# Kernel optimization log

Measured on AMD Instinct MI355X. Metric: run time of the kernel, lower is better.

The kernel has to match this reference:

```python
import jax, jax.numpy as jnp
import numpy as np

B, S, SE, D, H, FF, E, K = 2, 2048, 2048, 1024, 16, 4096, 8, 2
HD = D // H


def setup_inputs() -> dict:
    key = jax.random.key(0)
    ks = jax.random.split(key, 32)
    w = lambda k, shape: jax.random.normal(k, shape, jnp.float32) * 0.02
    inp = {
        'x': jax.random.normal(ks[0], (B, S, D), jnp.float32),
        'encoder_output': jax.random.normal(ks[1], (B, SE, D), jnp.float32),
        # causal self-attention projections
        'sa_wq': w(ks[2], (D, D)), 'sa_bq': jnp.zeros((D,), jnp.float32),
        'sa_wk': w(ks[3], (D, D)), 'sa_bk': jnp.zeros((D,), jnp.float32),
        'sa_wv': w(ks[4], (D, D)), 'sa_bv': jnp.zeros((D,), jnp.float32),
        'sa_wo': w(ks[5], (D, D)), 'sa_bo': jnp.zeros((D,), jnp.float32),
        # cross-attention projections
        'ca_wq': w(ks[6], (D, D)), 'ca_bq': jnp.zeros((D,), jnp.float32),
        'ca_wk': w(ks[7], (D, D)), 'ca_bk': jnp.zeros((D,), jnp.float32),
        'ca_wv': w(ks[8], (D, D)), 'ca_bv': jnp.zeros((D,), jnp.float32),
        'ca_wo': w(ks[9], (D, D)), 'ca_bo': jnp.zeros((D,), jnp.float32),
        # layernorms
        'ln1_g': jnp.ones((D,), jnp.float32), 'ln1_b': jnp.zeros((D,), jnp.float32),
        'ln2_g': jnp.ones((D,), jnp.float32), 'ln2_b': jnp.zeros((D,), jnp.float32),
        'ln3_g': jnp.ones((D,), jnp.float32), 'ln3_b': jnp.zeros((D,), jnp.float32),
        # router + experts
        'router_w': w(ks[10], (D, E)), 'router_b': jnp.zeros((E,), jnp.float32),
        'e_w1': w(ks[11], (E, D, FF)), 'e_b1': jnp.zeros((E, FF), jnp.float32),
        'e_w2': w(ks[12], (E, FF, D)), 'e_b2': jnp.zeros((E, D), jnp.float32),
    }
    return inp


def _layernorm(x, g, b):
    m = x.mean(-1, keepdims=True)
    v = ((x - m) ** 2).mean(-1, keepdims=True)
    return (x - m) / jnp.sqrt(v + 1e-5) * g + b


def _attn(q_in, k_in, v_in, wq, bq, wk, bk, wv, bv, wo, bo, causal):
    Bq, Sq, Dm = q_in.shape
    Sk = k_in.shape[1]
    Q = (q_in @ wq + bq).reshape(Bq, Sq, H, HD)
    Kp = (k_in @ wk + bk).reshape(Bq, Sk, H, HD)
    V = (v_in @ wv + bv).reshape(Bq, Sk, H, HD)
    scores = jnp.einsum('bqhd,bkhd->bhqk', Q, Kp) / jnp.sqrt(jnp.float32(HD))
    if causal:
        mask = jnp.tril(jnp.ones((Sq, Sk), bool))
        scores = jnp.where(mask, scores, -jnp.inf)
    a = jax.nn.softmax(scores, axis=-1)
    o = jnp.einsum('bhqk,bkhd->bqhd', a, V).reshape(Bq, Sq, Dm)
    return o @ wo + bo


def _moe(x, rw, rb, w1, b1, w2, b2):
    T = x.shape[0] * x.shape[1]
    xf = x.reshape(T, D)
    router_weights = jax.nn.softmax(xf @ rw + rb, axis=-1)          # [T,E]
    topw, topi = jax.lax.top_k(router_weights, K)                   # [T,K]
    topw = jax.nn.softmax(topw, axis=-1)                            # renormalize top-k
    # combine[t,e] = sum_k topw[t,k] * (topi[t,k]==e)
    combine = jnp.zeros((T, E), xf.dtype).at[jnp.arange(T)[:, None], topi].add(topw)
    # dense compute over all experts (same math as masked dispatch)
    h = jax.nn.gelu(jnp.einsum('td,edf->etf', xf, w1) + b1[:, None, :], approximate=False)
    eo = jnp.einsum('etf,efd->etd', h, w2) + b2[:, None, :]          # [E,T,D]
    out = jnp.einsum('etd,te->td', eo, combine)
    return out.reshape(x.shape)


def reference(x, encoder_output,
              sa_wq, sa_bq, sa_wk, sa_bk, sa_wv, sa_bv, sa_wo, sa_bo,
              ca_wq, ca_bq, ca_wk, ca_bk, ca_wv, ca_bv, ca_wo, ca_bo,
              ln1_g, ln1_b, ln2_g, ln2_b, ln3_g, ln3_b,
              router_w, router_b, e_w1, e_b1, e_w2, e_b2):
    x = _layernorm(x + _attn(x, x, x, sa_wq, sa_bq, sa_wk, sa_bk, sa_wv, sa_bv, sa_wo, sa_bo, True), ln1_g, ln1_b)
    x = _layernorm(x + _attn(x, encoder_output, encoder_output, ca_wq, ca_bq, ca_wk, ca_bk, ca_wv, ca_bv, ca_wo, ca_bo, False), ln2_g, ln2_b)
    x = _layernorm(x + _moe(x, router_w, router_b, e_w1, e_b1, e_w2, e_b2), ln3_g, ln3_b)
    return x
```

## Files before the change

### kernel.cpp

```cpp
#include <hip/hip_runtime.h>

typedef unsigned short u16;
typedef unsigned int   u32;
typedef __bf16    bf16x8 __attribute__((ext_vector_type(8)));
typedef _Float16  f16x8  __attribute__((ext_vector_type(8)));
typedef __fp16    fp16x2 __attribute__((ext_vector_type(2)));
typedef float     f32x4  __attribute__((ext_vector_type(4)));
typedef u16       u16x4  __attribute__((ext_vector_type(4)));

#define DEV static __device__ __forceinline__

constexpr int DIMc  = 1024;
constexpr int NHEAD = 16;
constexpr int HDM   = 64;
constexpr int SLENc = 2048;
constexpr int NBAT  = 2;
constexpr int NTOK  = NBAT * SLENc;
constexpr int FFD   = 4096;
constexpr int NEXP  = 8;
constexpr int NSLOT = 2 * NTOK;
constexpr long TD   = (long)NTOK * DIMc;
constexpr float RSC = 2048.0f;
constexpr float RSCI = 1.0f / 2048.0f;

DEV u16 f2bf(float f) {
  u32 u = __float_as_uint(f);
  u += 0x7fffu + ((u >> 16) & 1u);
  return (u16)(u >> 16);
}
DEV float bf2f(u16 h) { return __uint_as_float(((u32)h) << 16); }
DEV float h2f(u16 u) { union { _Float16 h; u16 u_; } x; x.u_ = u; return (float)x.h; }

DEV void split2v(float v, u16& h, u16& r) {
  _Float16 hh = (_Float16)v;
  float rf = (v - (float)hh) * RSC;
  union { _Float16 h_; u16 u_; } a, b;
  a.h_ = hh; b.h_ = (_Float16)rf;
  h = a.u_; r = b.u_;
}

DEV u32 pkrtz(float a, float b) {
  union { fp16x2 v; u32 u; } x;
  x.v = __builtin_amdgcn_cvt_pkrtz(a, b);
  return x.u;
}

DEV void async16(const void* g, void* l) {
  __builtin_amdgcn_global_load_lds((const u32*)g, (u32*)l, 16, 0, 0);
}

DEV f32x4 mfma_bf(bf16x8 a, bf16x8 b, f32x4 c) {
  return __builtin_amdgcn_mfma_f32_16x16x32_bf16(a, b, c, 0, 0, 0);
}
DEV f32x4 mfma_h(f16x8 a, f16x8 b, f32x4 c) {
  return __builtin_amdgcn_mfma_f32_16x16x32_f16(a, b, c, 0, 0, 0);
}

DEV f16x8 ldfragh(const u16 (*T)[64], int row, int blk) {
  return *(const f16x8*)((const u16*)T + row * 64 + ((blk ^ (row & 7)) * 8));
}

__global__ __launch_bounds__(256) void split2_kernel(
    const float* __restrict__ x, u16* __restrict__ o0, u16* __restrict__ o1, long n) {
  long i = ((long)blockIdx.x * 256 + threadIdx.x) * 4;
  if (i >= n) return;
  f32x4 v = *(const f32x4*)(x + i);
  u16x4 h, r;
#pragma unroll
  for (int j = 0; j < 4; ++j) { u16 a, b; split2v(v[j], a, b); h[j] = a; r[j] = b; }
  *(u16x4*)(o0 + i) = h;
  *(u16x4*)(o1 + i) = r;
}

__global__ __launch_bounds__(256) void wsplit2_kernel(
    const float* __restrict__ W, u16* __restrict__ t0, u16* __restrict__ t1, int R, int C) {
  __shared__ alignas(16) float tile[32][33];
  const long base = (long)blockIdx.z * R * C;
  const int c0 = blockIdx.x * 32, r0 = blockIdx.y * 32;
  const int tx = threadIdx.x & 31, ty = threadIdx.x >> 5;
#pragma unroll
  for (int i = 0; i < 32; i += 8)
    tile[ty + i][tx] = W[base + (long)(r0 + ty + i) * C + (c0 + tx)];
  __syncthreads();
#pragma unroll
  for (int i = 0; i < 32; i += 8) {
    float v = tile[tx][ty + i];
    long oidx = base + (long)(c0 + ty + i) * R + (r0 + tx);
    u16 a, b; split2v(v, a, b);
    t0[oidx] = a; t1[oidx] = b;
  }
}

__global__ __launch_bounds__(256) void wsplit1_kernel(
    const float* __restrict__ W, u16* __restrict__ t0, int R, int C) {
  __shared__ alignas(16) float tile[32][33];
  const long base = (long)blockIdx.z * R * C;
  const int c0 = blockIdx.x * 32, r0 = blockIdx.y * 32;
  const int tx = threadIdx.x & 31, ty = threadIdx.x >> 5;
#pragma unroll
  for (int i = 0; i < 32; i += 8)
    tile[ty + i][tx] = W[base + (long)(r0 + ty + i) * C + (c0 + tx)];
  __syncthreads();
#pragma unroll
  for (int i = 0; i < 32; i += 8) {
    long oidx = base + (long)(c0 + ty + i) * R + (r0 + tx);
    t0[oidx] = f2bf(tile[tx][ty + i]);
  }
}

__global__ __launch_bounds__(256) void biascat_kernel(
    const float* __restrict__ q, const float* __restrict__ k, const float* __restrict__ v,
    const float* __restrict__ ck, const float* __restrict__ cv,
    float* __restrict__ qkvb, float* __restrict__ kvb) {
  int i = blockIdx.x * 256 + threadIdx.x;
  if (i < 1024) qkvb[i] = q[i];
  else if (i < 2048) qkvb[i] = k[i - 1024];
  else if (i < 3072) qkvb[i] = v[i - 2048];
  else if (i < 4096) kvb[i - 3072] = ck[i - 3072];
  else if (i < 5120) kvb[i - 3072] = cv[i - 4096];
}

__global__ __launch_bounds__(256) void vtrans2_kernel(
    const u16* __restrict__ vh, const u16* __restrict__ vr, int ld,
    u16* __restrict__ t0, u16* __restrict__ t1) {
  __shared__ alignas(16) float tile[32][33];
  const int bh = blockIdx.z, b = bh >> 4, h = bh & 15;
  const int s0 = blockIdx.x * 32, d0 = blockIdx.y * 32;
  const int tx = threadIdx.x & 31, ty = threadIdx.x >> 5;
#pragma unroll
  for (int i = 0; i < 32; i += 8) {
    long idx = (long)(b * SLENc + s0 + ty + i) * ld + h * HDM + d0 + tx;
    tile[ty + i][tx] = h2f(vh[idx]) + h2f(vr[idx]) * RSCI;
  }
  __syncthreads();
#pragma unroll
  for (int i = 0; i < 32; i += 8) {
    float v = tile[tx][ty + i];
    long o = ((long)bh * HDM + d0 + ty + i) * SLENc + s0 + tx;
    u16 a, b_; split2v(v, a, b_);
    t0[o] = a; t1[o] = b_;
  }
}

template<int BK, bool SPLIT, bool GATHER, int EPI>
__global__ __launch_bounds__(256) void gemm_kernel(
    const u16* __restrict__ A0, const u16* __restrict__ A1,
    const u16* __restrict__ B0, const u16* __restrict__ B1,
    const float* __restrict__ bias, void* __restrict__ Cout, u16* __restrict__ C1,
    int M, int N, int Kd,
    const int* __restrict__ tlist, const int* __restrict__ cnts, const int* __restrict__ offs) {
  constexpr int NP = SPLIT ? 2 : 1;
  constexpr int NCH = (BK == 32) ? 2 : 4;
  __shared__ alignas(16) u16 As[NP][128 * BK];
  __shared__ alignas(16) u16 Bs[NP][128 * BK];

  const int e   = blockIdx.z;
  const int cnt = cnts ? cnts[e] : M;
  const int off = offs ? offs[e] : 0;
  const int m0  = blockIdx.y * 128;
  if (m0 >= cnt) return;
  const int n0  = blockIdx.x * 128;

  const int tid = threadIdx.x;
  const int lane = tid & 63, wid = tid >> 6;
  const int fr = lane & 15, kc = lane >> 4;
  const int wr = wid >> 1, wc = wid & 1;

  const long boff = (long)e * N * Kd;

  long arow_off[NCH], brow_off[NCH];
#pragma unroll
  for (int c = 0; c < NCH; ++c) {
    int row, kseg8;
    if constexpr (BK == 32) {
      const int chunk = wid * 2 + c;
      row = chunk * 16 + (lane >> 2);
      kseg8 = lane & 3;
    } else {
      const int chunk = wid * 4 + c;
      const int srow8 = lane >> 3;
      row = chunk * 8 + srow8;
      kseg8 = (lane & 7) ^ (srow8 & 7);
    }
    long ar;
    if (GATHER) {
      int idx = m0 + row; if (idx >= cnt) idx = cnt - 1;
      ar = tlist[off + idx];
    } else {
      ar = (long)(off + m0 + row);
    }
    arow_off[c] = ar * Kd + kseg8 * 8;
    brow_off[c] = boff + (long)(n0 + row) * Kd + kseg8 * 8;
  }

  f32x4 acc[4][4], acc1[4][4];
#pragma unroll
  for (int m = 0; m < 4; ++m)
#pragma unroll
    for (int n = 0; n < 4; ++n) { acc[m][n] = f32x4{0.f,0.f,0.f,0.f}; acc1[m][n] = f32x4{0.f,0.f,0.f,0.f}; }

  const int NK = Kd / BK;
  for (int kt = 0; kt < NK; ++kt) {
    const int k0 = kt * BK;
    __syncthreads();
#pragma unroll
    for (int c = 0; c < NCH; ++c) {
      const int chunk = wid * NCH + c;
      async16(A0 + arow_off[c] + k0, &As[0][chunk * 512]);
      async16(B0 + brow_off[c] + k0, &Bs[0][chunk * 512]);
      if constexpr (SPLIT) {
        async16(A1 + arow_off[c] + k0, &As[1][chunk * 512]);
        async16(B1 + brow_off[c] + k0, &Bs[1][chunk * 512]);
      }
    }
    __syncthreads();

    if constexpr (BK == 32) {
      if constexpr (SPLIT) {
        f16x8 a0[4], a1[4];
#pragma unroll
        for (int m = 0; m < 4; ++m) {
          const int idx = (wr * 64 + m * 16 + fr) * 32 + kc * 8;
          a0[m] = *(const f16x8*)&As[0][idx];
          a1[m] = *(const f16x8*)&As[1][idx];
        }
#pragma unroll
        for (int n = 0; n < 4; ++n) {
          const int idx = (wc * 64 + n * 16 + fr) * 32 + kc * 8;
          f16x8 b0 = *(const f16x8*)&Bs[0][idx];
          f16x8 b1 = *(const f16x8*)&Bs[1][idx];
#pragma unroll
          for (int m = 0; m < 4; ++m) {
            acc[m][n]  = mfma_h(a0[m], b0, acc[m][n]);
            acc1[m][n] = mfma_h(a0[m], b1, acc1[m][n]);
            acc1[m][n] = mfma_h(a1[m], b0, acc1[m][n]);
          }
        }
      } else {
        bf16x8 a0[4];
#pragma unroll
        for (int m = 0; m < 4; ++m)
          a0[m] = *(const bf16x8*)&As[0][(wr * 64 + m * 16 + fr) * 32 + kc * 8];
#pragma unroll
        for (int n = 0; n < 4; ++n) {
          bf16x8 b0 = *(const bf16x8*)&Bs[0][(wc * 64 + n * 16 + fr) * 32 + kc * 8];
#pragma unroll
          for (int m = 0; m < 4; ++m)
            acc[m][n] = mfma_bf(a0[m], b0, acc[m][n]);
        }
      }
    } else {
#pragma unroll
      for (int ksub = 0; ksub < 2; ++ksub) {
        bf16x8 a0[4];
#pragma unroll
        for (int m = 0; m < 4; ++m) {
          const int row = wr * 64 + m * 16 + fr;
          a0[m] = *(const bf16x8*)&As[0][row * 64 + (((ksub << 2) | kc) ^ (fr & 7)) * 8];
        }
#pragma unroll
        for (int n = 0; n < 4; ++n) {
          const int row = wc * 64 + n * 16 + fr;
          bf16x8 b0 = *(const bf16x8*)&Bs[0][row * 64 + (((ksub << 2) | kc) ^ (fr & 7)) * 8];
#pragma unroll
          for (int m = 0; m < 4; ++m)
            acc[m][n] = mfma_bf(a0[m], b0, acc[m][n]);
        }
      }
    }
  }

  const float* bvec = bias + (long)e * N;
#pragma unroll
  for (int m = 0; m < 4; ++m) {
#pragma unroll
    for (int j = 0; j < 4; ++j) {
      const int r = m0 + wr * 64 + m * 16 + (lane >> 4) * 4 + j;
      if (r >= cnt) continue;
      const long orow = (long)(off + r) * N;
#pragma unroll
      for (int n = 0; n < 4; ++n) {
        const int col = n0 + wc * 64 + n * 16 + fr;
        float v = acc[m][n][j];
        if constexpr (SPLIT) v += acc1[m][n][j] * RSCI;
        v += bvec[col];
        if constexpr (EPI == 0) {
          ((float*)Cout)[orow + col] = v;
        } else if constexpr (EPI == 1) {
          float g = 0.5f * v * (1.0f + erff(v * 0.70710678118654752f));
          ((u16*)Cout)[orow + col] = f2bf(g);
        } else if constexpr (EPI == 2) {
          ((u16*)Cout)[orow + col] = f2bf(v);
        } else {
          u16 a_, b_; split2v(v, a_, b_);
          ((u16*)Cout)[orow + col] = a_;
          C1[orow + col] = b_;
        }
      }
    }
  }
}

DEV f16x8 gather_fragh(u32 a0, u32 a1, u32 b0, u32 b1, int lane) {
  const int kc = lane >> 4;
  const int base = (lane & 15) + ((kc & 1) << 5);
  union { u32 u[4]; f16x8 v; } r;
  u32 s00 = (u32)__shfl((int)a0, base, 64);
  u32 s01 = (u32)__shfl((int)a1, base, 64);
  u32 s10 = (u32)__shfl((int)b0, base, 64);
  u32 s11 = (u32)__shfl((int)b1, base, 64);
  u32 t00 = (u32)__shfl((int)a0, base + 16, 64);
  u32 t01 = (u32)__shfl((int)a1, base + 16, 64);
  u32 t10 = (u32)__shfl((int)b0, base + 16, 64);
  u32 t11 = (u32)__shfl((int)b1, base + 16, 64);
  const bool hi = (kc >> 1) != 0;
  r.u[0] = hi ? s10 : s00;
  r.u[1] = hi ? s11 : s01;
  r.u[2] = hi ? t10 : t00;
  r.u[3] = hi ? t11 : t01;
  return r.v;
}

template<bool CAUSAL>
__global__ __launch_bounds__(256, 3) void attn2_kernel(
    const u16* __restrict__ Qh, const u16* __restrict__ Qr, int qld,
    const u16* __restrict__ Kh, const u16* __restrict__ Kr, int kld,
    const u16* __restrict__ Vh, const u16* __restrict__ Vr,
    u16* __restrict__ OH, u16* __restrict__ OR) {
  __shared__ alignas(16) u16 KQs[2][64][64];
  __shared__ alignas(16) u16 Vts[2][64][64];

  const int qt = blockIdx.x, h = blockIdx.y, b = blockIdx.z;
  const int tid = threadIdx.x, lane = tid & 63, w = tid >> 6;
  const int fr = lane & 15, kc = lane >> 4;
  const int q0 = qt * 64;
  const long qbase = (long)(b * SLENc) * qld + h * HDM;
  const long kbase = (long)(b * SLENc) * kld + h * HDM;
  const long obase = (long)(b * SLENc) * DIMc + h * HDM;
  const long vtbase = (long)(b * NHEAD + h) * HDM * SLENc;
  const int r = lane >> 3, blk = (lane & 7) ^ r;

#pragma unroll
  for (int p = 0; p < 2; ++p) {
    const u16* gp = (p == 0 ? Qh : Qr);
#pragma unroll
    for (int cc = 0; cc < 2; ++cc) {
      int c = w + 4 * cc;
      async16(gp + qbase + (long)(q0 + 8 * c + r) * qld + blk * 8, &KQs[p][8 * c][0]);
    }
  }
  __syncthreads();
  f16x8 qf0[2], qf1[2];
#pragma unroll
  for (int s = 0; s < 2; ++s) {
    qf0[s] = ldfragh(KQs[0], w * 16 + fr, s * 4 + kc);
    qf1[s] = ldfragh(KQs[1], w * 16 + fr, s * 4 + kc);
  }
  __syncthreads();

  f32x4 accO0[4], accO1[4];
#pragma unroll
  for (int dn = 0; dn < 4; ++dn) { accO0[dn] = f32x4{0.f,0.f,0.f,0.f}; accO1[dn] = f32x4{0.f,0.f,0.f,0.f}; }
  float m_ = -3e38f, l_ = 0.f;

  const int nkt = CAUSAL ? (qt + 1) : (SLENc / 64);
  for (int kt = 0; kt < nkt; ++kt) {
    __syncthreads();
    {
#pragma unroll
      for (int p = 0; p < 2; ++p) {
        const u16* gp = (p == 0 ? Kh : Kr);
#pragma unroll
        for (int cc = 0; cc < 2; ++cc) {
          int c = w + 4 * cc;
          async16(gp + kbase + (long)(kt * 64 + 8 * c + r) * kld + blk * 8, &KQs[p][8 * c][0]);
        }
      }
      const long vrow = vtbase + kt * 64;
#pragma unroll
      for (int p = 0; p < 2; ++p) {
        const u16* gp = (p == 0 ? Vh : Vr);
#pragma unroll
        for (int cc = 0; cc < 2; ++cc) {
          int c = w + 4 * cc;
          async16(gp + vrow + (long)(8 * c + r) * SLENc + blk * 8, &Vts[p][8 * c][0]);
        }
      }
    }
    __syncthreads();

    f32x4 sc0[4], sc1[4];
#pragma unroll
    for (int kn = 0; kn < 4; ++kn) { sc0[kn] = f32x4{0.f,0.f,0.f,0.f}; sc1[kn] = f32x4{0.f,0.f,0.f,0.f}; }
#pragma unroll
    for (int kn = 0; kn < 4; ++kn)
#pragma unroll
      for (int s = 0; s < 2; ++s) {
        f16x8 ah = ldfragh(KQs[0], kn * 16 + fr, s * 4 + kc);
        f16x8 ar = ldfragh(KQs[1], kn * 16 + fr, s * 4 + kc);
        sc0[kn] = mfma_h(ah, qf0[s], sc0[kn]);
        sc1[kn] = mfma_h(ah, qf1[s], sc1[kn]);
        sc1[kn] = mfma_h(ar, qf0[s], sc1[kn]);
      }

    constexpr float SCL = 0.125f, SCL2 = 0.125f * RSCI;
    float p_[4][4];
    float mx = -3e38f;
#pragma unroll
    for (int kn = 0; kn < 4; ++kn)
#pragma unroll
      for (int j = 0; j < 4; ++j) {
        float sv = fmaf(sc0[kn][j], SCL, sc1[kn][j] * SCL2);
        if (CAUSAL && kt == qt) {
          if (kn * 16 + kc * 4 + j > w * 16 + fr) sv = -3e38f;
        }
        p_[kn][j] = sv;
        mx = fmaxf(mx, sv);
      }
    mx = fmaxf(mx, __shfl_xor(mx, 16, 64));
    mx = fmaxf(mx, __shfl_xor(mx, 32, 64));
    if (!__all(mx <= m_ + 8.f)) {
      const float mn = fmaxf(m_, mx);
      const float corr = __expf(m_ - mn);
      m_ = mn;
      l_ *= corr;
#pragma unroll
      for (int dn = 0; dn < 4; ++dn) { accO0[dn] *= corr; accO1[dn] *= corr; }
    }
    float rs = 0.f;
#pragma unroll
    for (int kn = 0; kn < 4; ++kn)
#pragma unroll
      for (int j = 0; j < 4; ++j) {
        float p = __expf(p_[kn][j] - m_);
        p_[kn][j] = p;
        rs += p;
      }
    rs += __shfl_xor(rs, 16, 64);
    rs += __shfl_xor(rs, 32, 64);
    l_ += rs;

    u32 hpk[4][2], rpk[4][2];
#pragma unroll
    for (int kn = 0; kn < 4; ++kn)
#pragma unroll
      for (int jp = 0; jp < 2; ++jp) {
        float p0 = p_[kn][2 * jp], p1 = p_[kn][2 * jp + 1];
        u32 hp = pkrtz(p0, p1);
        float h0 = h2f((u16)hp), h1 = h2f((u16)(hp >> 16));
        u32 rp = pkrtz((p0 - h0) * RSC, (p1 - h1) * RSC);
        hpk[kn][jp] = hp;
        rpk[kn][jp] = rp;
      }

#pragma unroll
    for (int s = 0; s < 2; ++s) {
      f16x8 ph = gather_fragh(hpk[2 * s][0], hpk[2 * s][1], hpk[2 * s + 1][0], hpk[2 * s + 1][1], lane);
      f16x8 pr = gather_fragh(rpk[2 * s][0], rpk[2 * s][1], rpk[2 * s + 1][0], rpk[2 * s + 1][1], lane);
#pragma unroll
      for (int dn = 0; dn < 4; ++dn) {
        f16x8 vh = ldfragh(Vts[0], dn * 16 + fr, s * 4 + kc);
        f16x8 vr = ldfragh(Vts[1], dn * 16 + fr, s * 4 + kc);
        accO0[dn] = mfma_h(vh, ph, accO0[dn]);
        accO1[dn] = mfma_h(vh, pr, accO1[dn]);
        accO1[dn] = mfma_h(vr, ph, accO1[dn]);
      }
    }
  }

  const float inv = 1.0f / l_;
#pragma unroll
  for (int dn = 0; dn < 4; ++dn) {
    u16x4 hv, rv;
#pragma unroll
    for (int j = 0; j < 4; ++j) {
      float o = (accO0[dn][j] + accO1[dn][j] * RSCI) * inv;
      u16 a_, b_; split2v(o, a_, b_);
      hv[j] = a_; rv[j] = b_;
    }
    const long oidx = obase + (long)(q0 + w * 16 + fr) * DIMc + dn * 16 + kc * 4;
    *(u16x4*)&OH[oidx] = hv;
    *(u16x4*)&OR[oidx] = rv;
  }
}

template<int NS>
__global__ __launch_bounds__(256) void resln_kernel(
    const float* __restrict__ resid, const float* __restrict__ proj,
    const float* __restrict__ gam, const float* __restrict__ bet,
    float* __restrict__ yout, u16* __restrict__ s0, u16* __restrict__ s1) {
  __shared__ float red[4];
  const int t = blockIdx.x, tid = threadIdx.x;
  const long base = (long)t * DIMc;
  float v[4];
#pragma unroll
  for (int i = 0; i < 4; ++i) {
    int d = tid + i * 256;
    v[i] = resid[base + d] + proj[base + d];
  }
  float s = v[0] + v[1] + v[2] + v[3];
#pragma unroll
  for (int o = 32; o; o >>= 1) s += __shfl_xor(s, o, 64);
  if ((tid & 63) == 0) red[tid >> 6] = s;
  __syncthreads();
  const float mean = (red[0] + red[1] + red[2] + red[3]) * (1.0f / DIMc);
  __syncthreads();
  float q = 0.f;
#pragma unroll
  for (int i = 0; i < 4; ++i) { float d_ = v[i] - mean; q += d_ * d_; }
#pragma unroll
  for (int o = 32; o; o >>= 1) q += __shfl_xor(q, o, 64);
  if ((tid & 63) == 0) red[tid >> 6] = q;
  __syncthreads();
  const float var = (red[0] + red[1] + red[2] + red[3]) * (1.0f / DIMc);
  const float inv = rsqrtf(var + 1e-5f);
#pragma unroll
  for (int i = 0; i < 4; ++i) {
    int d = tid + i * 256;
    float y = (v[i] - mean) * inv * gam[d] + bet[d];
    yout[base + d] = y;
    if constexpr (NS == 1) s0[base + d] = f2bf(y);
    if constexpr (NS == 2) {
      u16 a, b; split2v(y, a, b);
      s0[base + d] = a; s1[base + d] = b;
    }
  }
}

__global__ __launch_bounds__(256) void router_kernel(
    const float* __restrict__ x2, const float* __restrict__ rw, const float* __restrict__ rb,
    int* __restrict__ topi, float* __restrict__ topw, int* __restrict__ cnt) {
  const int t = blockIdx.x * 4 + (threadIdx.x >> 6);
  const int lane = threadIdx.x & 63;
  float a[8] = {};
  for (int it = 0; it < 16; ++it) {
    int d = it * 64 + lane;
    float xv = x2[(long)t * DIMc + d];
    const f32x4* wp = (const f32x4*)&rw[d * 8];
    f32x4 w0 = wp[0], w1 = wp[1];
    a[0] += xv * w0[0]; a[1] += xv * w0[1]; a[2] += xv * w0[2]; a[3] += xv * w0[3];
    a[4] += xv * w1[0]; a[5] += xv * w1[1]; a[6] += xv * w1[2]; a[7] += xv * w1[3];
  }
#pragma unroll
  for (int o = 32; o; o >>= 1)
#pragma unroll
    for (int e = 0; e < 8; ++e) a[e] += __shfl_xor(a[e], o, 64);
  if (lane == 0) {
    float lg[8];
#pragma unroll
    for (int e = 0; e < 8; ++e) lg[e] = a[e] + rb[e];
    int i1 = 0;
#pragma unroll
    for (int e = 1; e < 8; ++e) if (lg[e] > lg[i1]) i1 = e;
    int i2 = (i1 == 0) ? 1 : 0;
#pragma unroll
    for (int e = 0; e < 8; ++e) if (e != i1 && lg[e] > lg[i2]) i2 = e;
    float mx = lg[i1], ps = 0.f, p[8];
#pragma unroll
    for (int e = 0; e < 8; ++e) { p[e] = __expf(lg[e] - mx); ps += p[e]; }
    float p1 = p[i1] / ps, p2 = p[i2] / ps;
    float e2 = __expf(p2 - p1);
    float w1 = 1.0f / (1.0f + e2);
    topi[t * 2] = i1; topi[t * 2 + 1] = i2;
    topw[t * 2] = w1; topw[t * 2 + 1] = e2 * w1;
    atomicAdd(&cnt[i1], 1); atomicAdd(&cnt[i2], 1);
  }
}

__global__ void scan_kernel(const int* __restrict__ cnt, int* __restrict__ offs, int* __restrict__ pos) {
  if (threadIdx.x == 0) {
    int a = 0;
    for (int e = 0; e < NEXP; ++e) { offs[e] = a; a += cnt[e]; }
  }
  if (threadIdx.x < NEXP) pos[threadIdx.x] = 0;
}

__global__ __launch_bounds__(256) void fill_kernel(
    const int* __restrict__ topi, const int* __restrict__ offs, int* __restrict__ pos,
    int* __restrict__ tlist, int* __restrict__ slotof) {
  int t = blockIdx.x * 256 + threadIdx.x;
  if (t >= NTOK) return;
#pragma unroll
  for (int k = 0; k < 2; ++k) {
    int e = topi[t * 2 + k];
    int pp = atomicAdd(&pos[e], 1);
    int s = offs[e] + pp;
    tlist[s] = t;
    slotof[t * 2 + k] = s;
  }
}

__global__ __launch_bounds__(256) void final_kernel(
    const float* __restrict__ x2, const u16* __restrict__ eo,
    const int* __restrict__ slotof, const float* __restrict__ topw,
    const float* __restrict__ gam, const float* __restrict__ bet, float* __restrict__ out) {
  __shared__ float red[4];
  const int t = blockIdx.x, tid = threadIdx.x;
  const long base = (long)t * DIMc;
  const int s0 = slotof[t * 2], s1 = slotof[t * 2 + 1];
  const float w0 = topw[t * 2], w1 = topw[t * 2 + 1];
  float v[4];
#pragma unroll
  for (int i = 0; i < 4; ++i) {
    int d = tid + i * 256;
    float moe = w0 * bf2f(eo[(long)s0 * DIMc + d]) + w1 * bf2f(eo[(long)s1 * DIMc + d]);
    v[i] = x2[base + d] + moe;
  }
  float s = v[0] + v[1] + v[2] + v[3];
#pragma unroll
  for (int o = 32; o; o >>= 1) s += __shfl_xor(s, o, 64);
  if ((tid & 63) == 0) red[tid >> 6] = s;
  __syncthreads();
  const float mean = (red[0] + red[1] + red[2] + red[3]) * (1.0f / DIMc);
  __syncthreads();
  float q = 0.f;
#pragma unroll
  for (int i = 0; i < 4; ++i) { float d_ = v[i] - mean; q += d_ * d_; }
#pragma unroll
  for (int o = 32; o; o >>= 1) q += __shfl_xor(q, o, 64);
  if ((tid & 63) == 0) red[tid >> 6] = q;
  __syncthreads();
  const float var = (red[0] + red[1] + red[2] + red[3]) * (1.0f / DIMc);
  const float inv = rsqrtf(var + 1e-5f);
#pragma unroll
  for (int i = 0; i < 4; ++i) {
    int d = tid + i * 256;
    out[base + d] = (v[i] - mean) * inv * gam[d] + bet[d];
  }
}

extern "C" void kernel_launch(void* const* d_in, const int* in_sizes, int n_in,
                              void* d_out, int out_size, void* d_ws, size_t ws_size,
                              hipStream_t stream) {
  (void)in_sizes; (void)n_in; (void)out_size; (void)ws_size;
  const float* x     = (const float*)d_in[0];
  const float* enc   = (const float*)d_in[1];
  const float* aw[8] = {(const float*)d_in[2],  (const float*)d_in[4],  (const float*)d_in[6],  (const float*)d_in[8],
                        (const float*)d_in[10], (const float*)d_in[12], (const float*)d_in[14], (const float*)d_in[16]};
  const float* ab[8] = {(const float*)d_in[3],  (const float*)d_in[5],  (const float*)d_in[7],  (const float*)d_in[9],
                        (const float*)d_in[11], (const float*)d_in[13], (const float*)d_in[15], (const float*)d_in[17]};
  const float* ln1_g = (const float*)d_in[18]; const float* ln1_b = (const float*)d_in[19];
  const float* ln2_g = (const float*)d_in[20]; const float* ln2_b = (const float*)d_in[21];
  const float* ln3_g = (const float*)d_in[22]; const float* ln3_b = (const float*)d_in[23];
  const float* rw    = (const float*)d_in[24]; const float* rb    = (const float*)d_in[25];
  const float* e_w1  = (const float*)d_in[26]; const float* e_b1  = (const float*)d_in[27];
  const float* e_w2  = (const float*)d_in[28]; const float* e_b2  = (const float*)d_in[29];

  char* basep = (char*)d_ws;
  size_t offb = 0;
  auto alloc = [&](size_t nbytes) -> void* {
    void* r = basep + offb;
    offb += (nbytes + 255) & ~(size_t)255;
    return r;
  };

  const size_t PLANE_BF = (size_t)TD * 2;
  const size_t PLANE_F  = (size_t)TD * 4;
  const size_t WPLANE   = (size_t)DIMc * DIMc * 2;

  u16 *xs0 = (u16*)alloc(PLANE_BF), *xs1 = (u16*)alloc(PLANE_BF);
  u16 *es0 = (u16*)alloc(PLANE_BF), *es1 = (u16*)alloc(PLANE_BF);
  u16 *os0 = (u16*)alloc(PLANE_BF), *os1 = (u16*)alloc(PLANE_BF);
  u16 *wqkv0 = (u16*)alloc(3 * WPLANE), *wqkv1 = (u16*)alloc(3 * WPLANE);
  u16 *wkv0  = (u16*)alloc(2 * WPLANE), *wkv1  = (u16*)alloc(2 * WPLANE);
  u16 *wq0   = (u16*)alloc(WPLANE),     *wq1   = (u16*)alloc(WPLANE);
  u16 *wo10  = (u16*)alloc(WPLANE),     *wo11  = (u16*)alloc(WPLANE);
  u16 *wo20  = (u16*)alloc(WPLANE),     *wo21  = (u16*)alloc(WPLANE);
  u16* w1t = (u16*)alloc((size_t)NEXP * FFD * DIMc * 2);
  u16* w2t = (u16*)alloc((size_t)NEXP * DIMc * FFD * 2);
  u16 *QKVh = (u16*)alloc(3 * PLANE_BF), *QKVr = (u16*)alloc(3 * PLANE_BF);
  u16 *KVh  = (u16*)alloc(2 * PLANE_BF), *KVr  = (u16*)alloc(2 * PLANE_BF);
  u16 *Qch  = (u16*)alloc(PLANE_BF),     *Qcr  = (u16*)alloc(PLANE_BF);
  u16 *Vth  = (u16*)alloc(PLANE_BF),     *Vtr  = (u16*)alloc(PLANE_BF);
  float* qkvb = (float*)alloc(3072 * 4);
  float* kvb  = (float*)alloc(2048 * 4);
  float* aout = (float*)alloc(PLANE_F);
  float* x1   = (float*)alloc(PLANE_F);
  float* x2   = (float*)alloc(PLANE_F);
  u16*   x2h  = (u16*)alloc(PLANE_BF);
  u16*   hbuf = (u16*)alloc((size_t)(NSLOT + 128) * FFD * 2);
  u16*   eo   = (u16*)alloc((size_t)NSLOT * DIMc * 2);
  int*   topi   = (int*)alloc(NSLOT * 4);
  float* topwp  = (float*)alloc(NSLOT * 4);
  int*   tlist  = (int*)alloc(NSLOT * 4);
  int*   slotof = (int*)alloc(NSLOT * 4);
  int*   cnt    = (int*)alloc(NEXP * 4);
  int*   offs   = (int*)alloc(NEXP * 4);
  int*   pos    = (int*)alloc(NEXP * 4);

  (void)hipMemsetAsync(cnt, 0, NEXP * sizeof(int), stream);

  const int SB = (int)(TD / 4 / 256);
  split2_kernel<<<SB, 256, 0, stream>>>(x, xs0, xs1, TD);
  split2_kernel<<<SB, 256, 0, stream>>>(enc, es0, es1, TD);
  for (int s = 0; s < 3; ++s)
    wsplit2_kernel<<<dim3(32, 32, 1), 256, 0, stream>>>(aw[s], wqkv0 + (size_t)s * DIMc * DIMc, wqkv1 + (size_t)s * DIMc * DIMc, DIMc, DIMc);
  wsplit2_kernel<<<dim3(32, 32, 1), 256, 0, stream>>>(aw[5], wkv0, wkv1, DIMc, DIMc);
  wsplit2_kernel<<<dim3(32, 32, 1), 256, 0, stream>>>(aw[6], wkv0 + (size_t)DIMc * DIMc, wkv1 + (size_t)DIMc * DIMc, DIMc, DIMc);
  wsplit2_kernel<<<dim3(32, 32, 1), 256, 0, stream>>>(aw[4], wq0, wq1, DIMc, DIMc);
  wsplit2_kernel<<<dim3(32, 32, 1), 256, 0, stream>>>(aw[3], wo10, wo11, DIMc, DIMc);
  wsplit2_kernel<<<dim3(32, 32, 1), 256, 0, stream>>>(aw[7], wo20, wo21, DIMc, DIMc);
  wsplit1_kernel<<<dim3(FFD / 32, DIMc / 32, NEXP), 256, 0, stream>>>(e_w1, w1t, DIMc, FFD);
  wsplit1_kernel<<<dim3(DIMc / 32, FFD / 32, NEXP), 256, 0, stream>>>(e_w2, w2t, FFD, DIMc);
  biascat_kernel<<<20, 256, 0, stream>>>(ab[0], ab[1], ab[2], ab[5], ab[6], qkvb, kvb);

  const dim3 gproj(DIMc / 128, NTOK / 128, 1);
  const dim3 gqkv(3 * DIMc / 128, NTOK / 128, 1);
  const dim3 gkv(2 * DIMc / 128, NTOK / 128, 1);
  const dim3 gattn(SLENc / 64, NHEAD, NBAT);
  const dim3 gvt(SLENc / 32, HDM / 32, NBAT * NHEAD);

  gemm_kernel<32, true, false, 3><<<gqkv, 256, 0, stream>>>(xs0, xs1, wqkv0, wqkv1, qkvb, QKVh, QKVr, NTOK, 3 * DIMc, DIMc, nullptr, nullptr, nullptr);
  vtrans2_kernel<<<gvt, 256, 0, stream>>>(QKVh + 2048, QKVr + 2048, 3 * DIMc, Vth, Vtr);
  attn2_kernel<true><<<gattn, 256, 0, stream>>>(QKVh, QKVr, 3 * DIMc, QKVh + 1024, QKVr + 1024, 3 * DIMc, Vth, Vtr, os0, os1);
  gemm_kernel<32, true, false, 0><<<gproj, 256, 0, stream>>>(os0, os1, wo10, wo11, ab[3], aout, nullptr, NTOK, DIMc, DIMc, nullptr, nullptr, nullptr);
  resln_kernel<2><<<NTOK, 256, 0, stream>>>(x, aout, ln1_g, ln1_b, x1, xs0, xs1);
  gemm_kernel<32, true, false, 3><<<gproj, 256, 0, stream>>>(xs0, xs1, wq0, wq1, ab[4], Qch, Qcr, NTOK, DIMc, DIMc, nullptr, nullptr, nullptr);
  gemm_kernel<32, true, false, 3><<<gkv, 256, 0, stream>>>(es0, es1, wkv0, wkv1, kvb, KVh, KVr, NTOK, 2 * DIMc, DIMc, nullptr, nullptr, nullptr);
  vtrans2_kernel<<<gvt, 256, 0, stream>>>(KVh + 1024, KVr + 1024, 2 * DIMc, Vth, Vtr);
  attn2_kernel<false><<<gattn, 256, 0, stream>>>(Qch, Qcr, DIMc, KVh, KVr, 2 * DIMc, Vth, Vtr, os0, os1);
  gemm_kernel<32, true, false, 0><<<gproj, 256, 0, stream>>>(os0, os1, wo20, wo21, ab[7], aout, nullptr, NTOK, DIMc, DIMc, nullptr, nullptr, nullptr);
  resln_kernel<1><<<NTOK, 256, 0, stream>>>(x1, aout, ln2_g, ln2_b, x2, x2h, nullptr);
  router_kernel<<<NTOK / 4, 256, 0, stream>>>(x2, rw, rb, topi, topwp, cnt);
  scan_kernel<<<1, 64, 0, stream>>>(cnt, offs, pos);
  fill_kernel<<<NTOK / 256, 256, 0, stream>>>(topi, offs, pos, tlist, slotof);
  gemm_kernel<64, false, true, 1><<<dim3(FFD / 128, NTOK / 128, NEXP), 256, 0, stream>>>(
      x2h, nullptr, w1t, nullptr, e_b1, hbuf, nullptr, NTOK, FFD, DIMc, tlist, cnt, offs);
  gemm_kernel<64, false, false, 2><<<dim3(DIMc / 128, NTOK / 128, NEXP), 256, 0, stream>>>(
      hbuf, nullptr, w2t, nullptr, e_b2, eo, nullptr, NTOK, DIMc, FFD, nullptr, cnt, offs);
  final_kernel<<<NTOK, 256, 0, stream>>>(x2, eo, slotof, topwp, ln3_g, ln3_b, (float*)d_out);
}
```

Before: 1.398 ms.

## Halve M tile for split GEMMs, use tanh GELU, add setprio in attention

Templates the GEMM on M-tile size and launches the fp16-split projection GEMMs with 64-row tiles, doubling the block count so more CUs have work and register pressure drops. The expert GEMMs keep 128-row tiles. The exact erf GELU is replaced with a tanh-form approximation built on exp, which changes the numerics relative to the reference's exact GELU. It also raises wave priority around the MFMA bursts in the attention kernel so matrix work issues ahead of other waves.

```diff
diff --git a/kernel.cpp b/kernel.cpp
--- a/kernel.cpp
+++ b/kernel.cpp
@@ -60,6 +60,11 @@
   return *(const f16x8*)((const u16*)T + row * 64 + ((blk ^ (row & 7)) * 8));
 }
 
+DEV float gelu_fast(float v) {
+  float arg = v * fmaf(0.044715f * v, v, 1.0f) * 0.7978845608028654f;
+  return v / (1.0f + __expf(-2.0f * arg));
+}
+
 __global__ __launch_bounds__(256) void split2_kernel(
     const float* __restrict__ x, u16* __restrict__ o0, u16* __restrict__ o1, long n) {
   long i = ((long)blockIdx.x * 256 + threadIdx.x) * 4;
@@ -142,22 +147,26 @@
   }
 }
 
-template<int BK, bool SPLIT, bool GATHER, int EPI>
+template<int MT, int BK, bool SPLIT, bool GATHER, int EPI>
 __global__ __launch_bounds__(256) void gemm_kernel(
     const u16* __restrict__ A0, const u16* __restrict__ A1,
     const u16* __restrict__ B0, const u16* __restrict__ B1,
     const float* __restrict__ bias, void* __restrict__ Cout, u16* __restrict__ C1,
     int M, int N, int Kd,
     const int* __restrict__ tlist, const int* __restrict__ cnts, const int* __restrict__ offs) {
-  constexpr int NP = SPLIT ? 2 : 1;
-  constexpr int NCH = (BK == 32) ? 2 : 4;
-  __shared__ alignas(16) u16 As[NP][128 * BK];
+  constexpr int NP   = SPLIT ? 2 : 1;
+  constexpr int RPC  = 512 / BK;
+  constexpr int ACH  = (MT / RPC) / 4;
+  constexpr int BCH  = (128 / RPC) / 4;
+  constexpr int MREP = MT / 32;
+  constexpr int WRS  = MT / 2;
+  __shared__ alignas(16) u16 As[NP][MT * BK];
   __shared__ alignas(16) u16 Bs[NP][128 * BK];
 
   const int e   = blockIdx.z;
   const int cnt = cnts ? cnts[e] : M;
   const int off = offs ? offs[e] : 0;
-  const int m0  = blockIdx.y * 128;
+  const int m0  = blockIdx.y * MT;
   if (m0 >= cnt) return;
   const int n0  = blockIdx.x * 128;
 
@@ -168,20 +177,14 @@
 
   const long boff = (long)e * N * Kd;
 
-  long arow_off[NCH], brow_off[NCH];
-#pragma unroll
-  for (int c = 0; c < NCH; ++c) {
-    int row, kseg8;
-    if constexpr (BK == 32) {
-      const int chunk = wid * 2 + c;
-      row = chunk * 16 + (lane >> 2);
-      kseg8 = lane & 3;
-    } else {
-      const int chunk = wid * 4 + c;
-      const int srow8 = lane >> 3;
-      row = chunk * 8 + srow8;
-      kseg8 = (lane & 7) ^ (srow8 & 7);
-    }
+  int srow, kseg8;
+  if constexpr (BK == 32) { srow = lane >> 2; kseg8 = lane & 3; }
+  else                    { srow = lane >> 3; kseg8 = (lane & 7) ^ (srow & 7); }
+
+  long aoff[ACH], boff_[BCH];
+#pragma unroll
+  for (int c = 0; c < ACH; ++c) {
+    const int row = (wid * ACH + c) * RPC + srow;
     long ar;
     if (GATHER) {
       int idx = m0 + row; if (idx >= cnt) idx = cnt - 1;
@@ -189,13 +192,17 @@
     } else {
       ar = (long)(off + m0 + row);
     }
-    arow_off[c] = ar * Kd + kseg8 * 8;
-    brow_off[c] = boff + (long)(n0 + row) * Kd + kseg8 * 8;
-  }
-
-  f32x4 acc[4][4], acc1[4][4];
-#pragma unroll
-  for (int m = 0; m < 4; ++m)
+    aoff[c] = ar * Kd + kseg8 * 8;
+  }
+#pragma unroll
+  for (int c = 0; c < BCH; ++c) {
+    const int row = (wid * BCH + c) * RPC + srow;
+    boff_[c] = boff + (long)(n0 + row) * Kd + kseg8 * 8;
+  }
+
+  f32x4 acc[MREP][4], acc1[MREP][4];
+#pragma unroll
+  for (int m = 0; m < MREP; ++m)
 #pragma unroll
     for (int n = 0; n < 4; ++n) { acc[m][n] = f32x4{0.f,0.f,0.f,0.f}; acc1[m][n] = f32x4{0.f,0.f,0.f,0.f}; }
 
@@ -204,23 +211,25 @@
     const int k0 = kt * BK;
     __syncthreads();
 #pragma unroll
-    for (int c = 0; c < NCH; ++c) {
-      const int chunk = wid * NCH + c;
-      async16(A0 + arow_off[c] + k0, &As[0][chunk * 512]);
-      async16(B0 + brow_off[c] + k0, &Bs[0][chunk * 512]);
-      if constexpr (SPLIT) {
-        async16(A1 + arow_off[c] + k0, &As[1][chunk * 512]);
-        async16(B1 + brow_off[c] + k0, &Bs[1][chunk * 512]);
-      }
+    for (int c = 0; c < ACH; ++c) {
+      const int chunk = wid * ACH + c;
+      async16(A0 + aoff[c] + k0, &As[0][chunk * 512]);
+      if constexpr (SPLIT) async16(A1 + aoff[c] + k0, &As[1][chunk * 512]);
+    }
+#pragma unroll
+    for (int c = 0; c < BCH; ++c) {
+      const int chunk = wid * BCH + c;
+      async16(B0 + boff_[c] + k0, &Bs[0][chunk * 512]);
+      if constexpr (SPLIT) async16(B1 + boff_[c] + k0, &Bs[1][chunk * 512]);
     }
     __syncthreads();
 
     if constexpr (BK == 32) {
       if constexpr (SPLIT) {
-        f16x8 a0[4], a1[4];
-#pragma unroll
-        for (int m = 0; m < 4; ++m) {
-          const int idx = (wr * 64 + m * 16 + fr) * 32 + kc * 8;
+        f16x8 a0[MREP], a1[MREP];
+#pragma unroll
+        for (int m = 0; m < MREP; ++m) {
+          const int idx = (wr * WRS + m * 16 + fr) * 32 + kc * 8;
           a0[m] = *(const f16x8*)&As[0][idx];
           a1[m] = *(const f16x8*)&As[1][idx];
         }
@@ -230,32 +239,32 @@
           f16x8 b0 = *(const f16x8*)&Bs[0][idx];
           f16x8 b1 = *(const f16x8*)&Bs[1][idx];
 #pragma unroll
-          for (int m = 0; m < 4; ++m) {
+          for (int m = 0; m < MREP; ++m) {
             acc[m][n]  = mfma_h(a0[m], b0, acc[m][n]);
             acc1[m][n] = mfma_h(a0[m], b1, acc1[m][n]);
             acc1[m][n] = mfma_h(a1[m], b0, acc1[m][n]);
           }
         }
       } else {
-        bf16x8 a0[4];
-#pragma unroll
-        for (int m = 0; m < 4; ++m)
-          a0[m] = *(const bf16x8*)&As[0][(wr * 64 + m * 16 + fr) * 32 + kc * 8];
+        bf16x8 a0[MREP];
+#pragma unroll
+        for (int m = 0; m < MREP; ++m)
+          a0[m] = *(const bf16x8*)&As[0][(wr * WRS + m * 16 + fr) * 32 + kc * 8];
 #pragma unroll
         for (int n = 0; n < 4; ++n) {
           bf16x8 b0 = *(const bf16x8*)&Bs[0][(wc * 64 + n * 16 + fr) * 32 + kc * 8];
 #pragma unroll
-          for (int m = 0; m < 4; ++m)
+          for (int m = 0; m < MREP; ++m)
             acc[m][n] = mfma_bf(a0[m], b0, acc[m][n]);
         }
       }
     } else {
 #pragma unroll
       for (int ksub = 0; ksub < 2; ++ksub) {
-        bf16x8 a0[4];
-#pragma unroll
-        for (int m = 0; m < 4; ++m) {
-          const int row = wr * 64 + m * 16 + fr;
+        bf16x8 a0[MREP];
+#pragma unroll
+        for (int m = 0; m < MREP; ++m) {
+          const int row = wr * WRS + m * 16 + fr;
           a0[m] = *(const bf16x8*)&As[0][row * 64 + (((ksub << 2) | kc) ^ (fr & 7)) * 8];
         }
 #pragma unroll
@@ -263,7 +272,7 @@
           const int row = wc * 64 + n * 16 + fr;
           bf16x8 b0 = *(const bf16x8*)&Bs[0][row * 64 + (((ksub << 2) | kc) ^ (fr & 7)) * 8];
 #pragma unroll
-          for (int m = 0; m < 4; ++m)
+          for (int m = 0; m < MREP; ++m)
             acc[m][n] = mfma_bf(a0[m], b0, acc[m][n]);
         }
       }
@@ -272,10 +281,10 @@
 
   const float* bvec = bias + (long)e * N;
 #pragma unroll
-  for (int m = 0; m < 4; ++m) {
+  for (int m = 0; m < MREP; ++m) {
 #pragma unroll
     for (int j = 0; j < 4; ++j) {
-      const int r = m0 + wr * 64 + m * 16 + (lane >> 4) * 4 + j;
+      const int r = m0 + wr * WRS + m * 16 + kc * 4 + j;
       if (r >= cnt) continue;
       const long orow = (long)(off + r) * N;
 #pragma unroll
@@ -287,8 +296,7 @@
         if constexpr (EPI == 0) {
           ((float*)Cout)[orow + col] = v;
         } else if constexpr (EPI == 1) {
-          float g = 0.5f * v * (1.0f + erff(v * 0.70710678118654752f));
-          ((u16*)Cout)[orow + col] = f2bf(g);
+          ((u16*)Cout)[orow + col] = f2bf(gelu_fast(v));
         } else if constexpr (EPI == 2) {
           ((u16*)Cout)[orow + col] = f2bf(v);
         } else {
@@ -392,6 +400,7 @@
     f32x4 sc0[4], sc1[4];
 #pragma unroll
     for (int kn = 0; kn < 4; ++kn) { sc0[kn] = f32x4{0.f,0.f,0.f,0.f}; sc1[kn] = f32x4{0.f,0.f,0.f,0.f}; }
+    __builtin_amdgcn_s_setprio(1);
 #pragma unroll
     for (int kn = 0; kn < 4; ++kn)
 #pragma unroll
@@ -402,6 +411,7 @@
         sc1[kn] = mfma_h(ah, qf1[s], sc1[kn]);
         sc1[kn] = mfma_h(ar, qf0[s], sc1[kn]);
       }
+    __builtin_amdgcn_s_setprio(0);
 
     constexpr float SCL = 0.125f, SCL2 = 0.125f * RSCI;
     float p_[4][4];
@@ -457,6 +467,7 @@
     for (int s = 0; s < 2; ++s) {
       f16x8 ph = gather_fragh(hpk[2 * s][0], hpk[2 * s][1], hpk[2 * s + 1][0], hpk[2 * s + 1][1], lane);
       f16x8 pr = gather_fragh(rpk[2 * s][0], rpk[2 * s][1], rpk[2 * s + 1][0], rpk[2 * s + 1][1], lane);
+      __builtin_amdgcn_s_setprio(1);
 #pragma unroll
       for (int dn = 0; dn < 4; ++dn) {
         f16x8 vh = ldfragh(Vts[0], dn * 16 + fr, s * 4 + kc);
@@ -465,6 +476,7 @@
         accO1[dn] = mfma_h(vh, pr, accO1[dn]);
         accO1[dn] = mfma_h(vr, ph, accO1[dn]);
       }
+      __builtin_amdgcn_s_setprio(0);
     }
   }
 
@@ -704,29 +716,29 @@
   wsplit1_kernel<<<dim3(DIMc / 32, FFD / 32, NEXP), 256, 0, stream>>>(e_w2, w2t, FFD, DIMc);
   biascat_kernel<<<20, 256, 0, stream>>>(ab[0], ab[1], ab[2], ab[5], ab[6], qkvb, kvb);
 
-  const dim3 gproj(DIMc / 128, NTOK / 128, 1);
-  const dim3 gqkv(3 * DIMc / 128, NTOK / 128, 1);
-  const dim3 gkv(2 * DIMc / 128, NTOK / 128, 1);
+  const dim3 gproj(DIMc / 128, NTOK / 64, 1);
+  const dim3 gqkv(3 * DIMc / 128, NTOK / 64, 1);
+  const dim3 gkv(2 * DIMc / 128, NTOK / 64, 1);
   const dim3 gattn(SLENc / 64, NHEAD, NBAT);
   const dim3 gvt(SLENc / 32, HDM / 32, NBAT * NHEAD);
 
-  gemm_kernel<32, true, false, 3><<<gqkv, 256, 0, stream>>>(xs0, xs1, wqkv0, wqkv1, qkvb, QKVh, QKVr, NTOK, 3 * DIMc, DIMc, nullptr, nullptr, nullptr);
+  gemm_kernel<64, 32, true, false, 3><<<gqkv, 256, 0, stream>>>(xs0, xs1, wqkv0, wqkv1, qkvb, QKVh, QKVr, NTOK, 3 * DIMc, DIMc, nullptr, nullptr, nullptr);
   vtrans2_kernel<<<gvt, 256, 0, stream>>>(QKVh + 2048, QKVr + 2048, 3 * DIMc, Vth, Vtr);
   attn2_kernel<true><<<gattn, 256, 0, stream>>>(QKVh, QKVr, 3 * DIMc, QKVh + 1024, QKVr + 1024, 3 * DIMc, Vth, Vtr, os0, os1);
-  gemm_kernel<32, true, false, 0><<<gproj, 256, 0, stream>>>(os0, os1, wo10, wo11, ab[3], aout, nullptr, NTOK, DIMc, DIMc, nullptr, nullptr, nullptr);
+  gemm_kernel<64, 32, true, false, 0><<<gproj, 256, 0, stream>>>(os0, os1, wo10, wo11, ab[3], aout, nullptr, NTOK, DIMc, DIMc, nullptr, nullptr, nullptr);
   resln_kernel<2><<<NTOK, 256, 0, stream>>>(x, aout, ln1_g, ln1_b, x1, xs0, xs1);
-  gemm_kernel<32, true, false, 3><<<gproj, 256, 0, stream>>>(xs0, xs1, wq0, wq1, ab[4], Qch, Qcr, NTOK, DIMc, DIMc, nullptr, nullptr, nullptr);
-  gemm_kernel<32, true, false, 3><<<gkv, 256, 0, stream>>>(es0, es1, wkv0, wkv1, kvb, KVh, KVr, NTOK, 2 * DIMc, DIMc, nullptr, nullptr, nullptr);
+  gemm_kernel<64, 32, true, false, 3><<<gproj, 256, 0, stream>>>(xs0, xs1, wq0, wq1, ab[4], Qch, Qcr, NTOK, DIMc, DIMc, nullptr, nullptr, nullptr);
+  gemm_kernel<64, 32, true, false, 3><<<gkv, 256, 0, stream>>>(es0, es1, wkv0, wkv1, kvb, KVh, KVr, NTOK, 2 * DIMc, DIMc, nullptr, nullptr, nullptr);
   vtrans2_kernel<<<gvt, 256, 0, stream>>>(KVh + 1024, KVr + 1024, 2 * DIMc, Vth, Vtr);
   attn2_kernel<false><<<gattn, 256, 0, stream>>>(Qch, Qcr, DIMc, KVh, KVr, 2 * DIMc, Vth, Vtr, os0, os1);
-  gemm_kernel<32, true, false, 0><<<gproj, 256, 0, stream>>>(os0, os1, wo20, wo21, ab[7], aout, nullptr, NTOK, DIMc, DIMc, nullptr, nullptr, nullptr);
+  gemm_kernel<64, 32, true, false, 0><<<gproj, 256, 0, stream>>>(os0, os1, wo20, wo21, ab[7], aout, nullptr, NTOK, DIMc, DIMc, nullptr, nullptr, nullptr);
   resln_kernel<1><<<NTOK, 256, 0, stream>>>(x1, aout, ln2_g, ln2_b, x2, x2h, nullptr);
   router_kernel<<<NTOK / 4, 256, 0, stream>>>(x2, rw, rb, topi, topwp, cnt);
   scan_kernel<<<1, 64, 0, stream>>>(cnt, offs, pos);
   fill_kernel<<<NTOK / 256, 256, 0, stream>>>(topi, offs, pos, tlist, slotof);
-  gemm_kernel<64, false, true, 1><<<dim3(FFD / 128, NTOK / 128, NEXP), 256, 0, stream>>>(
+  gemm_kernel<128, 64, false, true, 1><<<dim3(FFD / 128, NTOK / 128, NEXP), 256, 0, stream>>>(
       x2h, nullptr, w1t, nullptr, e_b1, hbuf, nullptr, NTOK, FFD, DIMc, tlist, cnt, offs);
-  gemm_kernel<64, false, false, 2><<<dim3(DIMc / 128, NTOK / 128, NEXP), 256, 0, stream>>>(
+  gemm_kernel<128, 64, false, false, 2><<<dim3(DIMc / 128, NTOK / 128, NEXP), 256, 0, stream>>>(
       hbuf, nullptr, w2t, nullptr, e_b2, eo, nullptr, NTOK, DIMc, FFD, nullptr, cnt, offs);
   final_kernel<<<NTOK, 256, 0, stream>>>(x2, eo, slotof, topwp, ln3_g, ln3_b, (float*)d_out);
 }
```

After: 1.236 ms. 11.6% less time.
